# Kernel tuning notes

Hardware: AMD Instinct MI355X
Metric: run time of the kernel (lower is better)

## Reference

```python
import jax, jax.numpy as jnp
import numpy as np

N, Dx, Dt, M, K = 524288, 128, 64, 32, 8
SK, SS = 1.0, 1.0  # l2 regularization strengths (experts, gate)


def setup_inputs() -> dict:
    key = jax.random.key(0)
    ks = jax.random.split(key, 6)
    w = 0.02  # small weight scale keeps per-sample log-likelihoods in fp32 range
    return {
        "x": jax.random.normal(ks[0], (N, Dx), dtype=jnp.float32),
        "t": jax.random.normal(ks[1], (N, Dt), dtype=jnp.float32),
        "y": jax.random.normal(ks[2], (N, M), dtype=jnp.float32),
        "Wm": jax.random.normal(ks[3], (K, Dx, M), dtype=jnp.float32) * w,
        "bm": jnp.zeros((K, M), dtype=jnp.float32),
        "Wv": jax.random.normal(ks[4], (K, Dx, M), dtype=jnp.float32) * w,
        "bv": jnp.zeros((K, M), dtype=jnp.float32),
        "Wg": jax.random.normal(ks[5], (Dt, K), dtype=jnp.float32) * w,
        "bg": jnp.zeros((K,), dtype=jnp.float32),
    }


def reference(x, t, y, Wm, bm, Wv, bv, Wg, bg):
    # Gate: softmax Dense over t -> pi [N, K]
    pi = jax.nn.softmax(t @ Wg + bg, axis=1)
    # All K expert heads as one batched matmul (fused form of the Python loop)
    mean = jnp.einsum("nd,kdm->nkm", x, Wm) + bm      # [N, K, M]
    logvar = jnp.einsum("nd,kdm->nkm", x, Wv) + bv    # [N, K, M]
    half_log_2pi = 0.5 * jnp.float32(np.log(2.0 * np.pi))
    diff = y[:, None, :] - mean                        # [N, K, M]
    # Gaussian log-likelihood per sample per expert -> [N, K]
    ll = -jnp.sum(diff * diff / (2.0 * jnp.exp(logvar)) + half_log_2pi + 0.5 * logvar, axis=2)
    # Mixture likelihood, then NLL (matches original: sum_k pi_k * exp(ll_k))
    mix = jnp.sum(pi * jnp.exp(ll), axis=1)            # [N]
    # Keras l1_l2(l2=s) kernel regularizers (biases excluded)
    reg = SK * (jnp.sum(Wm * Wm) + jnp.sum(Wv * Wv)) + SS * jnp.sum(Wg * Wg)
    return -jnp.sum(jnp.log(mix)) + reg
```

## Files before the change

kernel.cpp:

```cpp
#include <hip/hip_runtime.h>
#include <hip/hip_bf16.h>


#define NN 524288
#define DX 128
#define DT 64
#define MDIM 32
#define KEXP 8
#define TILE_R 64
#define THREADS 1024
#define GRID_MAIN 512
#define TPB 16

typedef __bf16 bf16x8 __attribute__((ext_vector_type(8)));
typedef float f32x4 __attribute__((ext_vector_type(4)));
typedef long long i64;

__device__ __forceinline__ bf16x8 cvt8(const f32x4 a, const f32x4 b) {
  bf16x8 r;
  r[0] = (__bf16)a[0]; r[1] = (__bf16)a[1]; r[2] = (__bf16)a[2]; r[3] = (__bf16)a[3];
  r[4] = (__bf16)b[0]; r[5] = (__bf16)b[1]; r[6] = (__bf16)b[2]; r[7] = (__bf16)b[3];
  return r;
}
__device__ __forceinline__ i64 cvt8f8(const f32x4 a, const f32x4 b) {
  int p0 = __builtin_amdgcn_cvt_pk_fp8_f32(a[0], a[1], 0, 0);
  p0 = __builtin_amdgcn_cvt_pk_fp8_f32(a[2], a[3], p0, 1);
  int p1 = __builtin_amdgcn_cvt_pk_fp8_f32(b[0], b[1], 0, 0);
  p1 = __builtin_amdgcn_cvt_pk_fp8_f32(b[2], b[3], p1, 1);
  return (i64)(((unsigned long long)(unsigned)p1 << 32) | (unsigned)p0);
}

#define MFMA16(a, b, c) __builtin_amdgcn_mfma_f32_16x16x32_bf16(a, b, c, 0, 0, 0)
#define MFMA8(a, b, c)  __builtin_amdgcn_mfma_f32_16x16x32_fp8_fp8(a, b, c, 0, 0, 0)

#define B_LDS() do { \
  asm volatile("s_waitcnt lgkmcnt(0)" ::: "memory"); \
  __builtin_amdgcn_s_barrier(); \
  __builtin_amdgcn_sched_barrier(0); } while (0)

#define HL2PI 0.91893853320467274f

__global__ __launch_bounds__(THREADS, 4) void mdn_main(
    const float* __restrict__ x, const float* __restrict__ t,
    const float* __restrict__ y, const float* __restrict__ Wm,
    const float* __restrict__ bm, const float* __restrict__ Wv,
    const float* __restrict__ bv, const float* __restrict__ Wg,
    const float* __restrict__ bg, float* __restrict__ partials,
    float* __restrict__ out_atomic)
{
  __shared__ __align__(16) unsigned char  xs_l[2][TILE_R * DX];
  __shared__ __align__(16) unsigned short ts_l[2][TILE_R * DT];
  __shared__ __align__(16) float ys_l[2][TILE_R * MDIM];
  __shared__ __align__(16) unsigned short wg_lds[2 * 64 * 8];
  __shared__ __align__(16) float llp4[2][TILE_R * 68];
  __shared__ __align__(16) float glog[2][TILE_R * 8];
  __shared__ float red_s[16];

  const int tid = threadIdx.x;
  const int lane = tid & 63;
  const int wv = tid >> 6;
  const int l15 = lane & 15;
  const int lhi = lane >> 4;
  const int kx = wv & 7;
  const int hh = wv >> 3;

  const int xr = tid >> 4, xsl = tid & 15;
  const int x_src = xr * DX + ((xsl ^ (xr & 7)) << 3);
  const int x_dst = xr * 128 + (xsl << 3);
  const int tr = tid >> 3, tsl = tid & 7;
  const int t_src = tr * DT + ((tsl ^ (tr & 7)) << 3);
  const int t_dst = tr * 128 + (tsl << 4);
  const int uy = tid - 512;
  const int yr = uy >> 3, ysl = uy & 7;
  const int y_src = yr * MDIM + ((ysl ^ (yr & 7)) << 2);
  const int y_dst = yr * 128 + (ysl << 4);

  f32x4 sa, sb, ea, eb;
  auto issue = [&](int tile) {
    const float* xp = x + (size_t)tile * (TILE_R * DX) + x_src;
    sa = *(const f32x4*)xp;
    sb = *(const f32x4*)(xp + 4);
    if (tid < 512) {
      const float* tp = t + (size_t)tile * (TILE_R * DT) + t_src;
      ea = *(const f32x4*)tp;
      eb = *(const f32x4*)(tp + 4);
    } else {
      ea = *(const f32x4*)(y + (size_t)tile * (TILE_R * MDIM) + y_src);
    }
  };
  auto commit = [&](int buf) {
    *(i64*)((char*)xs_l[buf] + x_dst) = cvt8f8(sa, sb);
    if (tid < 512) *(bf16x8*)((char*)ts_l[buf] + t_dst) = cvt8(ea, eb);
    else           *(f32x4*)((char*)ys_l[buf] + y_dst) = ea;
  };

  const int first = blockIdx.x * TPB;
  issue(first);

  const f32x4 bmean = *(const f32x4*)&bm[kx * MDIM + hh * 16 + lhi * 4];
  const f32x4 blv   = *(const f32x4*)&bv[kx * MDIM + hh * 16 + lhi * 4];
  f32x4 bgv = {0.f, 0.f, 0.f, 0.f};
  if (wv < 4) bgv = *(const f32x4*)&bg[(lhi & 1) * 4];

  i64 bfrag[2][4];
  #pragma unroll
  for (int ct = 0; ct < 2; ++ct) {
    const float* W = (ct ? Wv : Wm) + (size_t)kx * (DX * MDIM);
    const int mcol = hh * 16 + l15;
    #pragma unroll
    for (int kk = 0; kk < 4; ++kk) {
      f32x4 wa, wb;
      #pragma unroll
      for (int i = 0; i < 4; ++i) {
        wa[i] = W[(kk * 32 + lhi * 8 + i) * MDIM + mcol];
        wb[i] = W[(kk * 32 + lhi * 8 + 4 + i) * MDIM + mcol];
      }
      bfrag[ct][kk] = cvt8f8(wa, wb);
    }
  }
  if (wv == 15) {
    #pragma unroll
    for (int kk = 0; kk < 2; ++kk) {
      bf16x8 tmp;
      #pragma unroll
      for (int i = 0; i < 8; ++i) {
        const int d = kk * 32 + lhi * 8 + i;
        tmp[i] = (__bf16)((l15 < KEXP) ? Wg[d * KEXP + l15] : 0.f);
      }
      *(bf16x8*)((char*)wg_lds + (kk * 64 + lane) * 16) = tmp;
    }
  }

  commit(0);
  B_LDS();

  float loss_acc = 0.f;

  auto do_lse = [&](int pb) {
    const int rr = (wv - 4) * 16 + l15;
    const f32x4 lgv = *(const f32x4*)&glog[pb][rr * 8 + (lhi & 1) * 4];
    const int kb = (lhi & 1) * 4;
    f32x4 a4;
    #pragma unroll
    for (int j = 0; j < 4; ++j) {
      const f32x4 pA = *(const f32x4*)&llp4[pb][rr * 68 + (kb + j) * 4];
      const f32x4 pB = *(const f32x4*)&llp4[pb][rr * 68 + 32 + (kb + j) * 4];
      const float s8 = pA[0] + pA[1] + pA[2] + pA[3]
                     + pB[0] + pB[1] + pB[2] + pB[3];
      a4[j] = lgv[j] - s8 - 32.0f * HL2PI;
    }
    float mg = fmaxf(fmaxf(lgv[0], lgv[1]), fmaxf(lgv[2], lgv[3]));
    float ma = fmaxf(fmaxf(a4[0], a4[1]), fmaxf(a4[2], a4[3]));
    mg = fmaxf(mg, __shfl_xor(mg, 16));
    ma = fmaxf(ma, __shfl_xor(ma, 16));
    float eg = __expf(lgv[0] - mg) + __expf(lgv[1] - mg)
             + __expf(lgv[2] - mg) + __expf(lgv[3] - mg);
    float ea2 = __expf(a4[0] - ma) + __expf(a4[1] - ma)
              + __expf(a4[2] - ma) + __expf(a4[3] - ma);
    eg += __shfl_xor(eg, 16);
    ea2 += __shfl_xor(ea2, 16);
    if (lhi == 0)
      loss_acc += (mg + __logf(eg)) - (ma + __logf(ea2));
  };

  for (int it = 0; it < TPB; ++it) {
    const int cur = it & 1;
    issue(first + ((it + 1 < TPB) ? it + 1 : it));

    if (it && wv >= 4 && wv < 8) do_lse(cur ^ 1);

    if (wv < 4) {
      const int rr = wv * 16 + l15;
      const int r7 = rr & 7;
      f32x4 g = {0.f, 0.f, 0.f, 0.f};
      #pragma unroll
      for (int kk = 0; kk < 2; ++kk) {
        const int s = (kk * 4 + lhi) ^ r7;
        const bf16x8 tf = *(const bf16x8*)((const char*)ts_l[cur] + rr * 128 + s * 16);
        const bf16x8 wf = *(const bf16x8*)((const char*)wg_lds + (kk * 64 + lane) * 16);
        g = MFMA16(wf, tf, g);
      }
      if (lhi < 2) {
        f32x4 lg;
        #pragma unroll
        for (int j = 0; j < 4; ++j) lg[j] = g[j] + bgv[j];
        *(f32x4*)&glog[cur][rr * 8 + lhi * 4] = lg;
      }
    }

    const unsigned char* xc = xs_l[cur];
    const float* yc = ys_l[cur];
    #pragma unroll
    for (int rt = 0; rt < 4; ++rt) {
      const int rr = rt * 16 + l15;
      const int r7 = rr & 7;
      f32x4 acc0 = bmean, acc1 = blv;
      #pragma unroll
      for (int kk = 0; kk < 4; ++kk) {
        const int s = (kk * 4 + lhi) ^ r7;
        const i64 af = *(const i64*)(xc + rr * 128 + s * 8);
        acc0 = MFMA8(bfrag[0][kk], af, acc0);
        acc1 = MFMA8(bfrag[1][kk], af, acc1);
      }
      const int sy = (hh * 4 + lhi) ^ r7;
      const f32x4 y4 = *(const f32x4*)&yc[rr * 32 + sy * 4];
      float part = 0.f;
      #pragma unroll
      for (int j = 0; j < 4; ++j) {
        const float d = y4[j] - acc0[j];
        part += d * d * (0.5f * __expf(-acc1[j])) + 0.5f * acc1[j];
      }
      llp4[cur][rr * 68 + hh * 32 + kx * 4 + lhi] = part;
    }

    commit(cur ^ 1);
    B_LDS();
  }
  if (wv >= 4 && wv < 8) do_lse((TPB - 1) & 1);

  loss_acc += __shfl_xor(loss_acc, 1);
  loss_acc += __shfl_xor(loss_acc, 2);
  loss_acc += __shfl_xor(loss_acc, 4);
  loss_acc += __shfl_xor(loss_acc, 8);
  loss_acc += __shfl_xor(loss_acc, 16);
  loss_acc += __shfl_xor(loss_acc, 32);
  if (lane == 0) red_s[wv] = loss_acc;
  __syncthreads();
  if (tid == 0) {
    float s = 0.f;
    #pragma unroll
    for (int w = 0; w < 16; ++w) s += red_s[w];
    if (partials) partials[blockIdx.x] = s;
    else atomicAdd(out_atomic, s);
  }
}

__global__ void mdn_reg(const float* __restrict__ Wm, const float* __restrict__ Wv,
                        const float* __restrict__ Wg, float* __restrict__ partials,
                        float* __restrict__ out_atomic)
{
  __shared__ float red[4];
  const int gid = blockIdx.x * 256 + threadIdx.x;
  const int stride = 64 * 256;
  float s = 0.f;
  for (int i = gid; i < DX * MDIM * KEXP; i += stride) { float w = Wm[i]; s += w * w; }
  for (int i = gid; i < DX * MDIM * KEXP; i += stride) { float w = Wv[i]; s += w * w; }
  for (int i = gid; i < DT * KEXP; i += stride)        { float w = Wg[i]; s += w * w; }
  s += __shfl_xor(s, 1);
  s += __shfl_xor(s, 2);
  s += __shfl_xor(s, 4);
  s += __shfl_xor(s, 8);
  s += __shfl_xor(s, 16);
  s += __shfl_xor(s, 32);
  if ((threadIdx.x & 63) == 0) red[threadIdx.x >> 6] = s;
  __syncthreads();
  if (threadIdx.x == 0) {
    float b = red[0] + red[1] + red[2] + red[3];
    if (partials) partials[GRID_MAIN + blockIdx.x] = b;
    else atomicAdd(out_atomic, b);
  }
}

__global__ void mdn_final(const float* __restrict__ partials, float* __restrict__ out)
{
  __shared__ float red[4];
  float s = 0.f;
  for (int i = threadIdx.x; i < GRID_MAIN + 64; i += 256) s += partials[i];
  s += __shfl_xor(s, 1);
  s += __shfl_xor(s, 2);
  s += __shfl_xor(s, 4);
  s += __shfl_xor(s, 8);
  s += __shfl_xor(s, 16);
  s += __shfl_xor(s, 32);
  if ((threadIdx.x & 63) == 0) red[threadIdx.x >> 6] = s;
  __syncthreads();
  if (threadIdx.x == 0) out[0] = red[0] + red[1] + red[2] + red[3];
}

extern "C" void kernel_launch(void* const* d_in, const int* in_sizes, int n_in,
                              void* d_out, int out_size, void* d_ws, size_t ws_size,
                              hipStream_t stream)
{
  const float* x  = (const float*)d_in[0];
  const float* t  = (const float*)d_in[1];
  const float* y  = (const float*)d_in[2];
  const float* Wm = (const float*)d_in[3];
  const float* bm = (const float*)d_in[4];
  const float* Wv = (const float*)d_in[5];
  const float* bv = (const float*)d_in[6];
  const float* Wg = (const float*)d_in[7];
  const float* bg = (const float*)d_in[8];
  float* out = (float*)d_out;

  if (ws_size >= (GRID_MAIN + 64) * sizeof(float)) {
    float* partials = (float*)d_ws;
    mdn_main<<<GRID_MAIN, THREADS, 0, stream>>>(x, t, y, Wm, bm, Wv, bv, Wg, bg,
                                                partials, nullptr);
    mdn_reg<<<64, 256, 0, stream>>>(Wm, Wv, Wg, partials, nullptr);
    mdn_final<<<1, 256, 0, stream>>>(partials, out);
  } else {
    hipMemsetAsync(out, 0, sizeof(float), stream);
    mdn_main<<<GRID_MAIN, THREADS, 0, stream>>>(x, t, y, Wm, bm, Wv, bv, Wg, bg,
                                                nullptr, out);
    mdn_reg<<<64, 256, 0, stream>>>(Wm, Wv, Wg, nullptr, out);
  }
}
```

Baseline: 120.5 us.

## Warp-specialize: 8 compute waves per expert, 8 loader/gate/LSE waves, smaller tiles

Splits the 16 waves into roles. Waves 0-7 each own one expert and compute both output halves (four MFMA chains per row tile). Waves 8-15 handle global loads and fp8/bf16 conversion, with waves 8-9 doing the gate and waves 10-11 the log-sum-exp. The row tile halves to 32 and tiles per block double, and biases now come from LDS. The aim is to keep compute waves off the load and convert path. The cost is that only half the waves do the main MFMA work, and each holds twice as many weight fragments in registers.

```diff
diff --git a/kernel.cpp b/kernel.cpp
--- a/kernel.cpp
+++ b/kernel.cpp
@@ -7,10 +7,10 @@
 #define DT 64
 #define MDIM 32
 #define KEXP 8
-#define TILE_R 64
+#define TILE_R 32
 #define THREADS 1024
 #define GRID_MAIN 512
-#define TPB 16
+#define TPB 32
 
 typedef __bf16 bf16x8 __attribute__((ext_vector_type(8)));
 typedef float f32x4 __attribute__((ext_vector_type(4)));
@@ -52,7 +52,9 @@
   __shared__ __align__(16) unsigned short ts_l[2][TILE_R * DT];
   __shared__ __align__(16) float ys_l[2][TILE_R * MDIM];
   __shared__ __align__(16) unsigned short wg_lds[2 * 64 * 8];
-  __shared__ __align__(16) float llp4[2][TILE_R * 68];
+  __shared__ __align__(16) float bm_s[KEXP * MDIM];
+  __shared__ __align__(16) float bv_s[KEXP * MDIM];
+  __shared__ __align__(16) float llp4[2][TILE_R * 40];
   __shared__ __align__(16) float glog[2][TILE_R * 8];
   __shared__ float red_s[16];
 
@@ -61,26 +63,26 @@
   const int wv = tid >> 6;
   const int l15 = lane & 15;
   const int lhi = lane >> 4;
-  const int kx = wv & 7;
-  const int hh = wv >> 3;
-
-  const int xr = tid >> 4, xsl = tid & 15;
+
+  const int p = tid - 512;
+  const int xr = p >> 4, xsl = p & 15;
   const int x_src = xr * DX + ((xsl ^ (xr & 7)) << 3);
   const int x_dst = xr * 128 + (xsl << 3);
-  const int tr = tid >> 3, tsl = tid & 7;
+  const int tr = p >> 3, tsl = p & 7;
   const int t_src = tr * DT + ((tsl ^ (tr & 7)) << 3);
   const int t_dst = tr * 128 + (tsl << 4);
-  const int uy = tid - 512;
+  const int uy = p - 256;
   const int yr = uy >> 3, ysl = uy & 7;
   const int y_src = yr * MDIM + ((ysl ^ (yr & 7)) << 2);
   const int y_dst = yr * 128 + (ysl << 4);
 
   f32x4 sa, sb, ea, eb;
   auto issue = [&](int tile) {
+    if (tid < 512) return;
     const float* xp = x + (size_t)tile * (TILE_R * DX) + x_src;
     sa = *(const f32x4*)xp;
     sb = *(const f32x4*)(xp + 4);
-    if (tid < 512) {
+    if (p < 256) {
       const float* tp = t + (size_t)tile * (TILE_R * DT) + t_src;
       ea = *(const f32x4*)tp;
       eb = *(const f32x4*)(tp + 4);
@@ -89,33 +91,39 @@
     }
   };
   auto commit = [&](int buf) {
+    if (tid < 512) return;
     *(i64*)((char*)xs_l[buf] + x_dst) = cvt8f8(sa, sb);
-    if (tid < 512) *(bf16x8*)((char*)ts_l[buf] + t_dst) = cvt8(ea, eb);
-    else           *(f32x4*)((char*)ys_l[buf] + y_dst) = ea;
+    if (p < 256) *(bf16x8*)((char*)ts_l[buf] + t_dst) = cvt8(ea, eb);
+    else         *(f32x4*)((char*)ys_l[buf] + y_dst) = ea;
   };
 
   const int first = blockIdx.x * TPB;
   issue(first);
 
-  const f32x4 bmean = *(const f32x4*)&bm[kx * MDIM + hh * 16 + lhi * 4];
-  const f32x4 blv   = *(const f32x4*)&bv[kx * MDIM + hh * 16 + lhi * 4];
+  if (tid < KEXP * MDIM) bm_s[tid] = bm[tid];
+  else if (tid < 2 * KEXP * MDIM) bv_s[tid - KEXP * MDIM] = bv[tid - KEXP * MDIM];
   f32x4 bgv = {0.f, 0.f, 0.f, 0.f};
-  if (wv < 4) bgv = *(const f32x4*)&bg[(lhi & 1) * 4];
-
-  i64 bfrag[2][4];
-  #pragma unroll
-  for (int ct = 0; ct < 2; ++ct) {
-    const float* W = (ct ? Wv : Wm) + (size_t)kx * (DX * MDIM);
-    const int mcol = hh * 16 + l15;
+  if (wv == 8 || wv == 9) bgv = *(const f32x4*)&bg[(lhi & 1) * 4];
+
+  i64 bfrag[2][2][4];
+  if (wv < 8) {
     #pragma unroll
-    for (int kk = 0; kk < 4; ++kk) {
-      f32x4 wa, wb;
+    for (int ct = 0; ct < 2; ++ct) {
+      const float* W = (ct ? Wv : Wm) + (size_t)wv * (DX * MDIM);
       #pragma unroll
-      for (int i = 0; i < 4; ++i) {
-        wa[i] = W[(kk * 32 + lhi * 8 + i) * MDIM + mcol];
-        wb[i] = W[(kk * 32 + lhi * 8 + 4 + i) * MDIM + mcol];
+      for (int hh = 0; hh < 2; ++hh) {
+        const int mcol = hh * 16 + l15;
+        #pragma unroll
+        for (int kk = 0; kk < 4; ++kk) {
+          f32x4 wa, wb;
+          #pragma unroll
+          for (int i = 0; i < 4; ++i) {
+            wa[i] = W[(kk * 32 + lhi * 8 + i) * MDIM + mcol];
+            wb[i] = W[(kk * 32 + lhi * 8 + 4 + i) * MDIM + mcol];
+          }
+          bfrag[ct][hh][kk] = cvt8f8(wa, wb);
+        }
       }
-      bfrag[ct][kk] = cvt8f8(wa, wb);
     }
   }
   if (wv == 15) {
@@ -137,17 +145,14 @@
   float loss_acc = 0.f;
 
   auto do_lse = [&](int pb) {
-    const int rr = (wv - 4) * 16 + l15;
+    const int rr = (wv - 10) * 16 + l15;
     const f32x4 lgv = *(const f32x4*)&glog[pb][rr * 8 + (lhi & 1) * 4];
     const int kb = (lhi & 1) * 4;
     f32x4 a4;
     #pragma unroll
     for (int j = 0; j < 4; ++j) {
-      const f32x4 pA = *(const f32x4*)&llp4[pb][rr * 68 + (kb + j) * 4];
-      const f32x4 pB = *(const f32x4*)&llp4[pb][rr * 68 + 32 + (kb + j) * 4];
-      const float s8 = pA[0] + pA[1] + pA[2] + pA[3]
-                     + pB[0] + pB[1] + pB[2] + pB[3];
-      a4[j] = lgv[j] - s8 - 32.0f * HL2PI;
+      const f32x4 pq = *(const f32x4*)&llp4[pb][rr * 40 + (kb + j) * 4];
+      a4[j] = lgv[j] - (pq[0] + pq[1] + pq[2] + pq[3]) - 32.0f * HL2PI;
     }
     float mg = fmaxf(fmaxf(lgv[0], lgv[1]), fmaxf(lgv[2], lgv[3]));
     float ma = fmaxf(fmaxf(a4[0], a4[1]), fmaxf(a4[2], a4[3]));
@@ -167,56 +172,65 @@
     const int cur = it & 1;
     issue(first + ((it + 1 < TPB) ? it + 1 : it));
 
-    if (it && wv >= 4 && wv < 8) do_lse(cur ^ 1);
-
-    if (wv < 4) {
-      const int rr = wv * 16 + l15;
-      const int r7 = rr & 7;
-      f32x4 g = {0.f, 0.f, 0.f, 0.f};
+    if (wv < 8) {
+      const unsigned char* xc = xs_l[cur];
+      const float* yc = ys_l[cur];
       #pragma unroll
-      for (int kk = 0; kk < 2; ++kk) {
-        const int s = (kk * 4 + lhi) ^ r7;
-        const bf16x8 tf = *(const bf16x8*)((const char*)ts_l[cur] + rr * 128 + s * 16);
-        const bf16x8 wf = *(const bf16x8*)((const char*)wg_lds + (kk * 64 + lane) * 16);
-        g = MFMA16(wf, tf, g);
+      for (int rt = 0; rt < 2; ++rt) {
+        const int rr = rt * 16 + l15;
+        const int r7 = rr & 7;
+        f32x4 am0 = *(const f32x4*)&bm_s[wv * MDIM + lhi * 4];
+        f32x4 am1 = *(const f32x4*)&bm_s[wv * MDIM + 16 + lhi * 4];
+        f32x4 av0 = *(const f32x4*)&bv_s[wv * MDIM + lhi * 4];
+        f32x4 av1 = *(const f32x4*)&bv_s[wv * MDIM + 16 + lhi * 4];
+        #pragma unroll
+        for (int kk = 0; kk < 4; ++kk) {
+          const int s = (kk * 4 + lhi) ^ r7;
+          const i64 af = *(const i64*)(xc + rr * 128 + s * 8);
+          am0 = MFMA8(bfrag[0][0][kk], af, am0);
+          am1 = MFMA8(bfrag[0][1][kk], af, am1);
+          av0 = MFMA8(bfrag[1][0][kk], af, av0);
+          av1 = MFMA8(bfrag[1][1][kk], af, av1);
+        }
+        const int s0 = lhi ^ r7, s1 = (4 + lhi) ^ r7;
+        const f32x4 y0v = *(const f32x4*)&yc[rr * 32 + s0 * 4];
+        const f32x4 y1v = *(const f32x4*)&yc[rr * 32 + s1 * 4];
+        float part = 0.f;
+        #pragma unroll
+        for (int j = 0; j < 4; ++j) {
+          const float d0 = y0v[j] - am0[j];
+          const float d1 = y1v[j] - am1[j];
+          part += d0 * d0 * (0.5f * __expf(-av0[j])) + 0.5f * av0[j];
+          part += d1 * d1 * (0.5f * __expf(-av1[j])) + 0.5f * av1[j];
+        }
+        llp4[cur][rr * 40 + wv * 4 + lhi] = part;
       }
-      if (lhi < 2) {
-        f32x4 lg;
+    } else {
+      if (it && (wv == 10 || wv == 11)) do_lse(cur ^ 1);
+      if (wv == 8 || wv == 9) {
+        const int rr = (wv - 8) * 16 + l15;
+        const int r7 = rr & 7;
+        f32x4 g = {0.f, 0.f, 0.f, 0.f};
         #pragma unroll
-        for (int j = 0; j < 4; ++j) lg[j] = g[j] + bgv[j];
-        *(f32x4*)&glog[cur][rr * 8 + lhi * 4] = lg;
+        for (int kk = 0; kk < 2; ++kk) {
+          const int s = (kk * 4 + lhi) ^ r7;
+          const bf16x8 tf = *(const bf16x8*)((const char*)ts_l[cur] + rr * 128 + s * 16);
+          const bf16x8 wf = *(const bf16x8*)((const char*)wg_lds + (kk * 64 + lane) * 16);
+          g = MFMA16(wf, tf, g);
+        }
+        if (lhi < 2) {
+          f32x4 lg;
+          #pragma unroll
+          for (int j = 0; j < 4; ++j) lg[j] = g[j] + bgv[j];
+          *(f32x4*)&glog[cur][rr * 8 + lhi * 4] = lg;
+        }
       }
-    }
-
-    const unsigned char* xc = xs_l[cur];
-    const float* yc = ys_l[cur];
-    #pragma unroll
-    for (int rt = 0; rt < 4; ++rt) {
-      const int rr = rt * 16 + l15;
-      const int r7 = rr & 7;
-      f32x4 acc0 = bmean, acc1 = blv;
-      #pragma unroll
-      for (int kk = 0; kk < 4; ++kk) {
-        const int s = (kk * 4 + lhi) ^ r7;
-        const i64 af = *(const i64*)(xc + rr * 128 + s * 8);
-        acc0 = MFMA8(bfrag[0][kk], af, acc0);
-        acc1 = MFMA8(bfrag[1][kk], af, acc1);
-      }
-      const int sy = (hh * 4 + lhi) ^ r7;
-      const f32x4 y4 = *(const f32x4*)&yc[rr * 32 + sy * 4];
-      float part = 0.f;
-      #pragma unroll
-      for (int j = 0; j < 4; ++j) {
-        const float d = y4[j] - acc0[j];
-        part += d * d * (0.5f * __expf(-acc1[j])) + 0.5f * acc1[j];
-      }
-      llp4[cur][rr * 68 + hh * 32 + kx * 4 + lhi] = part;
-    }
-
-    commit(cur ^ 1);
+      commit(cur ^ 1);
+    }
+
     B_LDS();
   }
-  if (wv >= 4 && wv < 8) do_lse((TPB - 1) & 1);
+  if (wv == 10 || wv == 11) do_lse((TPB - 1) & 1);
 
   loss_acc += __shfl_xor(loss_acc, 1);
   loss_acc += __shfl_xor(loss_acc, 2);
```

Result: slower. 134.5 us (+11.7%).
